# Kernel optimization log

Hardware: AMD Instinct MI355X
Metric: run time of the kernel (lower is better)

## Reference

```python
import jax, jax.numpy as jnp
import numpy as np

MAX_REL_POS = 1024


def rel_to_abs(x):
    """Music Transformer skew: [b,h,l,l] rel logits -> abs-position logits."""
    b, h, l, _ = x.shape
    x = jnp.pad(x, ((0, 0), (0, 0), (0, 0), (1, 0)))  # pad left of last dim
    x = x.reshape(b, h, l + 1, l)
    return x[:, :, 1:l + 1, :l]


def get_rel_embeddings(embed, seq_len):
    m = embed.shape[0]
    pad_len = max(seq_len - m, 0)
    start = max(m - seq_len, 0)
    padded = jnp.pad(embed, ((pad_len, 0), (0, 0)))
    return padded[start:, :]  # [seq_len, d]


def setup_inputs() -> dict:
    key = jax.random.key(0)
    kq, kk, kv, kr = jax.random.split(key, 4)
    B, H, L, D = 2, 8, 2048, 64
    # scale q so logits are O(1) (realistic attention magnitudes)
    q = jax.random.normal(kq, (B, H, L, D), dtype=jnp.float32) * (1.0 / np.sqrt(D))
    k = jax.random.normal(kk, (B, H, L, D), dtype=jnp.float32)
    v = jax.random.normal(kv, (B, H, L, D), dtype=jnp.float32)
    rel_keys_weight = jax.random.normal(kr, (MAX_REL_POS, D), dtype=jnp.float32)
    # causal mask: True = masked (masked_fill semantics)
    mask = jnp.triu(jnp.ones((L, L), dtype=bool), k=1)[None, None]
    return {"q": q, "k": k, "v": v, "rel_keys_weight": rel_keys_weight, "mask": mask}


def reference(q, k, v, rel_keys_weight, mask):
    L = q.shape[2]
    logits = jnp.einsum('bhqd,bhkd->bhqk', q, k)
    rel_keys = get_rel_embeddings(rel_keys_weight, L)          # [L, D]
    rel_logits = jnp.einsum('bhqd,md->bhqm', q, rel_keys)      # [B,H,L,L]
    logits = logits + rel_to_abs(rel_logits)
    logits = jnp.where(mask, -jnp.inf, logits)
    weights = jax.nn.softmax(logits, axis=3)
    output = jnp.matmul(weights, v)
    return (output, weights)
```

## Files before the change

kernel.cpp:

```cpp
#include <hip/hip_runtime.h>
#include <hip/hip_bf16.h>

typedef short bf16x8 __attribute__((ext_vector_type(8)));
typedef float f32x4  __attribute__((ext_vector_type(4)));

#define SEQ  2048
#define HD   64
#define LDT  72
#define TSTR 84
#define PSTR 72
#define OUT0 (16 * SEQ * HD)

__device__ __forceinline__ short f2bf(float x) {
    unsigned u = __float_as_uint(x);
    unsigned r = u + 0x7fffu + ((u >> 16) & 1u);
    return (short)(r >> 16);
}
__device__ __forceinline__ float bf2f(short s) {
    return __uint_as_float(((unsigned)(unsigned short)s) << 16);
}

__device__ __forceinline__ void stage64(const float* __restrict__ src_base,
                                        short* __restrict__ dst, int tid) {
    const int r = tid >> 2, cg = tid & 3;
    const float4* src = (const float4*)(src_base + (size_t)r * HD + cg * 16);
    float f[16];
#pragma unroll
    for (int t = 0; t < 4; ++t) {
        float4 v4 = src[t];
        f[4*t] = v4.x; f[4*t+1] = v4.y; f[4*t+2] = v4.z; f[4*t+3] = v4.w;
    }
    bf16x8 p0, p1;
#pragma unroll
    for (int t = 0; t < 8; ++t) { p0[t] = f2bf(f[t]); p1[t] = f2bf(f[t+8]); }
    *(bf16x8*)&dst[r * LDT + cg * 16]     = p0;
    *(bf16x8*)&dst[r * LDT + cg * 16 + 8] = p1;
}

__device__ __forceinline__ void stageG(const float* __restrict__ eg,
                                       short* __restrict__ Gs, int tid, int i0, int j0) {
    const int dd = tid >> 1, hf = tid & 1;
    const int e = 1086 - i0 + j0 - dd;
    short* dst = &Gs[dd * LDT + hf * 32];
    if (e >= 0 && e < 1024) {
        const float4* src = (const float4*)(eg + (size_t)e * HD + hf * 32);
#pragma unroll
        for (int u = 0; u < 4; ++u) {
            float4 a = src[2*u], b = src[2*u + 1];
            bf16x8 p;
            p[0] = f2bf(a.x); p[1] = f2bf(a.y); p[2] = f2bf(a.z); p[3] = f2bf(a.w);
            p[4] = f2bf(b.x); p[5] = f2bf(b.y); p[6] = f2bf(b.z); p[7] = f2bf(b.w);
            *(bf16x8*)&dst[u * 8] = p;
        }
    } else {
        bf16x8 z = {0,0,0,0,0,0,0,0};
#pragma unroll
        for (int u = 0; u < 4; ++u) *(bf16x8*)&dst[u * 8] = z;
    }
}

__device__ __forceinline__ void compute_sc(const bf16x8* aq, const short* __restrict__ Ks,
                                           const short* __restrict__ Gs, short* __restrict__ Tw,
                                           int wv, int qd, int c, int i0, int j0, f32x4* sc) {
    f32x4 tc[5];
    const f32x4 zz = {0.f, 0.f, 0.f, 0.f};
#pragma unroll
    for (int ct = 0; ct < 4; ++ct) sc[ct] = zz;
#pragma unroll
    for (int dt = 0; dt < 5; ++dt) tc[dt] = zz;
#pragma unroll
    for (int s = 0; s < 2; ++s) {
        bf16x8 a = aq[s];
#pragma unroll
        for (int ct = 0; ct < 4; ++ct) {
            bf16x8 b = *(const bf16x8*)&Ks[(ct * 16 + c) * LDT + s * 32 + qd * 8];
            sc[ct] = __builtin_amdgcn_mfma_f32_16x16x32_bf16(a, b, sc[ct], 0, 0, 0);
        }
#pragma unroll
        for (int dt = 0; dt < 5; ++dt) {
            bf16x8 g = *(const bf16x8*)&Gs[((wv + dt) * 16 + c) * LDT + s * 32 + qd * 8];
            tc[dt] = __builtin_amdgcn_mfma_f32_16x16x32_bf16(a, g, tc[dt], 0, 0, 0);
        }
    }
#pragma unroll
    for (int dt = 0; dt < 5; ++dt)
#pragma unroll
        for (int rg = 0; rg < 4; ++rg)
            Tw[(qd * 4 + rg) * TSTR + dt * 16 + c] = f2bf(tc[dt][rg]);
#pragma unroll
    for (int ct = 0; ct < 4; ++ct)
#pragma unroll
        for (int rg = 0; rg < 4; ++rg) {
            const int rl  = qd * 4 + rg;
            const int ddl = rl + 63 - ct * 16 - c;
            float sval = sc[ct][rg] + bf2f(Tw[rl * TSTR + ddl]);
            const int ig = i0 + wv * 16 + rl;
            const int jg = j0 + ct * 16 + c;
            sc[ct][rg] = (jg <= ig) ? sval : -3.0e38f;
        }
}

__global__ __launch_bounds__(256, 2)
void relattn(const float* __restrict__ qg, const float* __restrict__ kg,
             const float* __restrict__ vg, const float* __restrict__ eg,
             float* __restrict__ outp)
{
    __shared__ short Qs[64 * LDT];
    __shared__ short Ks[64 * LDT];
    __shared__ short Vt[64 * LDT];
    __shared__ short Gs[128 * LDT];
    __shared__ short TP[4 * 16 * TSTR];

    const int tid  = threadIdx.x;
    const int wv   = tid >> 6;
    const int lane = tid & 63;
    const int qd   = lane >> 4;
    const int c    = lane & 15;

    const int bh = blockIdx.x & 15;
    const int qt = 31 - (blockIdx.x >> 4);
    const int i0 = qt * 64;

    float* Wg = outp + OUT0;

    {
        const int z0v = (qt + 1) * 16;
        for (int r = 0; r < 64; ++r) {
            float4* dst = (float4*)(Wg + ((size_t)(bh * SEQ + i0 + r)) * SEQ);
            for (int jv = z0v + tid; jv < SEQ / 4; jv += 256)
                dst[jv] = make_float4(0.f, 0.f, 0.f, 0.f);
        }
    }

    stage64(qg + ((size_t)(bh * SEQ + i0)) * HD, Qs, tid);
    __syncthreads();
    bf16x8 aq[2];
#pragma unroll
    for (int s = 0; s < 2; ++s)
        aq[s] = *(const bf16x8*)&Qs[(wv * 16 + c) * LDT + s * 32 + qd * 8];

    short* Tw = &TP[wv * 16 * TSTR];

    float mrun[4], lrun[4];
#pragma unroll
    for (int rg = 0; rg < 4; ++rg) { mrun[rg] = -3.0e38f; lrun[rg] = 0.f; }

    for (int kt = 0; kt <= qt; ++kt) {
        const int j0 = kt * 64;
        __syncthreads();
        stage64(kg + ((size_t)(bh * SEQ + j0)) * HD, Ks, tid);
        stageG(eg, Gs, tid, i0, j0);
        __syncthreads();

        f32x4 sc[4];
        compute_sc(aq, Ks, Gs, Tw, wv, qd, c, i0, j0, sc);

#pragma unroll
        for (int rg = 0; rg < 4; ++rg) {
            float mx = fmaxf(fmaxf(sc[0][rg], sc[1][rg]), fmaxf(sc[2][rg], sc[3][rg]));
            mx = fmaxf(mx, __shfl_xor(mx, 1));
            mx = fmaxf(mx, __shfl_xor(mx, 2));
            mx = fmaxf(mx, __shfl_xor(mx, 4));
            mx = fmaxf(mx, __shfl_xor(mx, 8));
            const float mnew = fmaxf(mrun[rg], mx);
            float ss = __expf(sc[0][rg] - mnew) + __expf(sc[1][rg] - mnew)
                     + __expf(sc[2][rg] - mnew) + __expf(sc[3][rg] - mnew);
            ss += __shfl_xor(ss, 1);
            ss += __shfl_xor(ss, 2);
            ss += __shfl_xor(ss, 4);
            ss += __shfl_xor(ss, 8);
            lrun[rg] = lrun[rg] * __expf(mrun[rg] - mnew) + ss;
            mrun[rg] = mnew;
        }
    }

    float linv[4];
#pragma unroll
    for (int rg = 0; rg < 4; ++rg) linv[rg] = 1.0f / lrun[rg];

    f32x4 ob[4];
    {
        const f32x4 zz = {0.f, 0.f, 0.f, 0.f};
#pragma unroll
        for (int dt = 0; dt < 4; ++dt) ob[dt] = zz;
    }

    for (int kt = 0; kt <= qt; ++kt) {
        const int j0 = kt * 64;
        __syncthreads();
        stage64(kg + ((size_t)(bh * SEQ + j0)) * HD, Ks, tid);
        stageG(eg, Gs, tid, i0, j0);
        {
            const int r = tid >> 2, cg = tid & 3;
            const float4* src = (const float4*)(vg + ((size_t)(bh * SEQ + j0 + r)) * HD + cg * 16);
            float f[16];
#pragma unroll
            for (int t = 0; t < 4; ++t) {
                float4 v4 = src[t];
                f[4*t] = v4.x; f[4*t+1] = v4.y; f[4*t+2] = v4.z; f[4*t+3] = v4.w;
            }
#pragma unroll
            for (int t = 0; t < 16; ++t) Vt[(cg * 16 + t) * LDT + r] = f2bf(f[t]);
        }
        __syncthreads();

        f32x4 sc[4];
        compute_sc(aq, Ks, Gs, Tw, wv, qd, c, i0, j0, sc);

#pragma unroll
        for (int rg = 0; rg < 4; ++rg) {
            const int rl = qd * 4 + rg;
            const int ig = i0 + wv * 16 + rl;
            float* wrow = Wg + ((size_t)(bh * SEQ + ig)) * SEQ + j0;
#pragma unroll
            for (int ct = 0; ct < 4; ++ct) {
                const float w = __expf(sc[ct][rg] - mrun[rg]) * linv[rg];
                wrow[ct * 16 + c] = w;
                Tw[rl * PSTR + ct * 16 + c] = f2bf(w);
            }
        }

#pragma unroll
        for (int s = 0; s < 2; ++s) {
            bf16x8 ap = *(const bf16x8*)&Tw[c * PSTR + s * 32 + qd * 8];
#pragma unroll
            for (int dt = 0; dt < 4; ++dt) {
                bf16x8 bv = *(const bf16x8*)&Vt[(dt * 16 + c) * LDT + s * 32 + qd * 8];
                ob[dt] = __builtin_amdgcn_mfma_f32_16x16x32_bf16(ap, bv, ob[dt], 0, 0, 0);
            }
        }
    }

#pragma unroll
    for (int dt = 0; dt < 4; ++dt)
#pragma unroll
        for (int rg = 0; rg < 4; ++rg) {
            const int ig = i0 + wv * 16 + qd * 4 + rg;
            outp[((size_t)(bh * SEQ + ig)) * HD + dt * 16 + c] = ob[dt][rg];
        }
}

extern "C" void kernel_launch(void* const* d_in, const int* in_sizes, int n_in,
                              void* d_out, int out_size, void* d_ws, size_t ws_size,
                              hipStream_t stream) {
    const float* q = (const float*)d_in[0];
    const float* k = (const float*)d_in[1];
    const float* v = (const float*)d_in[2];
    const float* e = (const float*)d_in[3];
    float* out = (float*)d_out;
    hipLaunchKernelGGL(relattn, dim3(512), dim3(256), 0, stream, q, k, v, e, out);
}
```

Before: 453.4 us.

## Precompute bf16 K/V^T/rel-embedding buffers and read operands directly from global

Adds a prep kernel that converts K, transposed V, and a padded rel-embedding table to bf16 in workspace. The attention kernel then drops its shared-memory staging and barriers and loads MFMA operands straight from global/L2. The skew of the relative logits is done with lane shuffles instead of a shared-memory round trip. The running max is removed and exp is taken without subtracting it, which relies on logits staying O(1). The q-tile order is changed to interleave long and short tiles across blocks. This risks overflow for large logits and uncoalesced global reads in exchange for fewer syncs and less LDS traffic.

```diff
diff --git a/kernel.cpp b/kernel.cpp
--- a/kernel.cpp
+++ b/kernel.cpp
@@ -1,115 +1,122 @@
 #include <hip/hip_runtime.h>
-#include <hip/hip_bf16.h>
 
 typedef short bf16x8 __attribute__((ext_vector_type(8)));
 typedef float f32x4  __attribute__((ext_vector_type(4)));
 
-#define SEQ  2048
-#define HD   64
-#define LDT  72
-#define TSTR 84
-#define PSTR 72
-#define OUT0 (16 * SEQ * HD)
+#define SEQ   2048
+#define HD    64
+#define OUT0  (16 * SEQ * HD)
+#define KB_OFF 0
+#define VT_OFF (16 * SEQ * HD)
+#define GT_OFF (2 * 16 * SEQ * HD)
+#define GPAD  1056
+#define GNR   2208
+#define PSTR  72
 
 __device__ __forceinline__ short f2bf(float x) {
     unsigned u = __float_as_uint(x);
     unsigned r = u + 0x7fffu + ((u >> 16) & 1u);
     return (short)(r >> 16);
 }
-__device__ __forceinline__ float bf2f(short s) {
-    return __uint_as_float(((unsigned)(unsigned short)s) << 16);
-}
-
-__device__ __forceinline__ void stage64(const float* __restrict__ src_base,
-                                        short* __restrict__ dst, int tid) {
-    const int r = tid >> 2, cg = tid & 3;
-    const float4* src = (const float4*)(src_base + (size_t)r * HD + cg * 16);
-    float f[16];
-#pragma unroll
-    for (int t = 0; t < 4; ++t) {
-        float4 v4 = src[t];
-        f[4*t] = v4.x; f[4*t+1] = v4.y; f[4*t+2] = v4.z; f[4*t+3] = v4.w;
-    }
-    bf16x8 p0, p1;
-#pragma unroll
-    for (int t = 0; t < 8; ++t) { p0[t] = f2bf(f[t]); p1[t] = f2bf(f[t+8]); }
-    *(bf16x8*)&dst[r * LDT + cg * 16]     = p0;
-    *(bf16x8*)&dst[r * LDT + cg * 16 + 8] = p1;
-}
-
-__device__ __forceinline__ void stageG(const float* __restrict__ eg,
-                                       short* __restrict__ Gs, int tid, int i0, int j0) {
-    const int dd = tid >> 1, hf = tid & 1;
-    const int e = 1086 - i0 + j0 - dd;
-    short* dst = &Gs[dd * LDT + hf * 32];
-    if (e >= 0 && e < 1024) {
-        const float4* src = (const float4*)(eg + (size_t)e * HD + hf * 32);
+__device__ __forceinline__ void cvt8(const float4& x, const float4& y, bf16x8& p) {
+    p[0] = f2bf(x.x); p[1] = f2bf(x.y); p[2] = f2bf(x.z); p[3] = f2bf(x.w);
+    p[4] = f2bf(y.x); p[5] = f2bf(y.y); p[6] = f2bf(y.z); p[7] = f2bf(y.w);
+}
+
+__global__ __launch_bounds__(256)
+void prep(const float* __restrict__ kg, const float* __restrict__ vg,
+          const float* __restrict__ eg, short* __restrict__ ws)
+{
+    const int b = blockIdx.x, t = threadIdx.x;
+    short* Kb = ws + KB_OFF;
+    short* Vt = ws + VT_OFF;
+    short* Gt = ws + GT_OFF;
+    if (b < 512) {
+        __shared__ short tile[64 * 72];
+        const int bh = b >> 5, kb = b & 31;
+        const int r = t >> 2, cg = t & 3;
+        const float4* src = (const float4*)(vg + ((size_t)(bh * SEQ + kb * 64 + r)) * HD + cg * 16);
+        bf16x8 p0, p1;
+        cvt8(src[0], src[1], p0);
+        cvt8(src[2], src[3], p1);
+        *(bf16x8*)&tile[r * 72 + cg * 16]     = p0;
+        *(bf16x8*)&tile[r * 72 + cg * 16 + 8] = p1;
+        __syncthreads();
+        const int d = t >> 2, kq = t & 3;
+#pragma unroll
+        for (int u = 0; u < 2; ++u) {
+            bf16x8 q;
+#pragma unroll
+            for (int x = 0; x < 8; ++x) q[x] = tile[(kq * 16 + u * 8 + x) * 72 + d];
+            *(bf16x8*)&Vt[((size_t)(bh * 64 + d)) * SEQ + kb * 64 + kq * 16 + u * 8] = q;
+        }
+    } else if (b < 768) {
+        const int idx = (b - 512) * 256 + t;
+        const float4* src = (const float4*)kg + (size_t)idx * 8;
+        short* dst = Kb + (size_t)idx * 32;
 #pragma unroll
         for (int u = 0; u < 4; ++u) {
-            float4 a = src[2*u], b = src[2*u + 1];
-            bf16x8 p;
-            p[0] = f2bf(a.x); p[1] = f2bf(a.y); p[2] = f2bf(a.z); p[3] = f2bf(a.w);
-            p[4] = f2bf(b.x); p[5] = f2bf(b.y); p[6] = f2bf(b.z); p[7] = f2bf(b.w);
+            bf16x8 p; cvt8(src[2 * u], src[2 * u + 1], p);
             *(bf16x8*)&dst[u * 8] = p;
         }
     } else {
-        bf16x8 z = {0,0,0,0,0,0,0,0};
-#pragma unroll
-        for (int u = 0; u < 4; ++u) *(bf16x8*)&dst[u * 8] = z;
-    }
-}
-
-__device__ __forceinline__ void compute_sc(const bf16x8* aq, const short* __restrict__ Ks,
-                                           const short* __restrict__ Gs, short* __restrict__ Tw,
-                                           int wv, int qd, int c, int i0, int j0, f32x4* sc) {
+        for (int i = (b - 768) * 256 + t; i < GNR * HD; i += 64 * 256) {
+            const int g = i >> 6, d = i & 63;
+            const int e = g - GPAD;
+            Gt[i] = (e >= 0 && e < 1024) ? f2bf(eg[(size_t)e * HD + d]) : (short)0;
+        }
+    }
+}
+
+__device__ __forceinline__ void compute_sc(const bf16x8* aq, const short* __restrict__ Kb,
+                                           const short* __restrict__ Gt,
+                                           int j0, int iw, int qd, int c, int lane,
+                                           f32x4* sc, bool diag, int dloc)
+{
     f32x4 tc[5];
     const f32x4 zz = {0.f, 0.f, 0.f, 0.f};
 #pragma unroll
     for (int ct = 0; ct < 4; ++ct) sc[ct] = zz;
 #pragma unroll
     for (int dt = 0; dt < 5; ++dt) tc[dt] = zz;
+    const short* kbase = Kb + ((size_t)(j0 + c)) * HD + qd * 8;
+    const short* gbase = Gt + ((size_t)(2142 + j0 - iw - c)) * HD + qd * 8;
 #pragma unroll
     for (int s = 0; s < 2; ++s) {
         bf16x8 a = aq[s];
 #pragma unroll
         for (int ct = 0; ct < 4; ++ct) {
-            bf16x8 b = *(const bf16x8*)&Ks[(ct * 16 + c) * LDT + s * 32 + qd * 8];
+            bf16x8 b = *(const bf16x8*)&kbase[(ct * 16) * HD + s * 32];
             sc[ct] = __builtin_amdgcn_mfma_f32_16x16x32_bf16(a, b, sc[ct], 0, 0, 0);
         }
 #pragma unroll
         for (int dt = 0; dt < 5; ++dt) {
-            bf16x8 g = *(const bf16x8*)&Gs[((wv + dt) * 16 + c) * LDT + s * 32 + qd * 8];
+            bf16x8 g = *(const bf16x8*)&gbase[-(dt * 16) * HD + s * 32];
             tc[dt] = __builtin_amdgcn_mfma_f32_16x16x32_bf16(a, g, tc[dt], 0, 0, 0);
         }
     }
 #pragma unroll
-    for (int dt = 0; dt < 5; ++dt)
-#pragma unroll
-        for (int rg = 0; rg < 4; ++rg)
-            Tw[(qd * 4 + rg) * TSTR + dt * 16 + c] = f2bf(tc[dt][rg]);
-#pragma unroll
-    for (int ct = 0; ct < 4; ++ct)
-#pragma unroll
-        for (int rg = 0; rg < 4; ++rg) {
-            const int rl  = qd * 4 + rg;
-            const int ddl = rl + 63 - ct * 16 - c;
-            float sval = sc[ct][rg] + bf2f(Tw[rl * TSTR + ddl]);
-            const int ig = i0 + wv * 16 + rl;
-            const int jg = j0 + ct * 16 + c;
-            sc[ct][rg] = (jg <= ig) ? sval : -3.0e38f;
-        }
+    for (int rg = 0; rg < 4; ++rg) {
+        const int rl  = qd * 4 + rg;
+        const int cp  = (rl + 63 - c) & 15;
+        const int src = (lane & 48) | cp;
+        const bool hi = (rl + 63 - cp) >= 64;
+#pragma unroll
+        for (int ct = 0; ct < 4; ++ct) {
+            float vs = hi ? tc[4 - ct][rg] : tc[3 - ct][rg];
+            float tr = __shfl(vs, src, 64);
+            float sval = sc[ct][rg] + tr;
+            if (diag && (ct * 16 + c > dloc + rl)) sval = -3.0e38f;
+            sc[ct][rg] = sval;
+        }
+    }
 }
 
 __global__ __launch_bounds__(256, 2)
-void relattn(const float* __restrict__ qg, const float* __restrict__ kg,
-             const float* __restrict__ vg, const float* __restrict__ eg,
+void relattn(const float* __restrict__ qg, const short* __restrict__ ws,
              float* __restrict__ outp)
 {
-    __shared__ short Qs[64 * LDT];
-    __shared__ short Ks[64 * LDT];
-    __shared__ short Vt[64 * LDT];
-    __shared__ short Gs[128 * LDT];
-    __shared__ short TP[4 * 16 * TSTR];
+    __shared__ short Ps[4 * 16 * PSTR];
 
     const int tid  = threadIdx.x;
     const int wv   = tid >> 6;
@@ -118,9 +125,14 @@
     const int c    = lane & 15;
 
     const int bh = blockIdx.x & 15;
-    const int qt = 31 - (blockIdx.x >> 4);
+    const int u  = blockIdx.x >> 4;
+    const int qt = (u < 16) ? (31 - u) : (u - 16);
     const int i0 = qt * 64;
-
+    const int iw = i0 + wv * 16;
+
+    const short* Kb = ws + KB_OFF + (size_t)bh * SEQ * HD;
+    const short* Vt = ws + VT_OFF + (size_t)bh * 64 * SEQ;
+    const short* Gt = ws + GT_OFF;
     float* Wg = outp + OUT0;
 
     {
@@ -132,51 +144,37 @@
         }
     }
 
-    stage64(qg + ((size_t)(bh * SEQ + i0)) * HD, Qs, tid);
-    __syncthreads();
     bf16x8 aq[2];
-#pragma unroll
-    for (int s = 0; s < 2; ++s)
-        aq[s] = *(const bf16x8*)&Qs[(wv * 16 + c) * LDT + s * 32 + qd * 8];
-
-    short* Tw = &TP[wv * 16 * TSTR];
-
-    float mrun[4], lrun[4];
-#pragma unroll
-    for (int rg = 0; rg < 4; ++rg) { mrun[rg] = -3.0e38f; lrun[rg] = 0.f; }
-
+    {
+        const float* qrow = qg + ((size_t)(bh * SEQ + iw + c)) * HD;
+#pragma unroll
+        for (int s = 0; s < 2; ++s) {
+            float4 x = *(const float4*)(qrow + s * 32 + qd * 8);
+            float4 y = *(const float4*)(qrow + s * 32 + qd * 8 + 4);
+            cvt8(x, y, aq[s]);
+        }
+    }
+
+    float lrun[4];
+#pragma unroll
+    for (int rg = 0; rg < 4; ++rg) lrun[rg] = 0.f;
     for (int kt = 0; kt <= qt; ++kt) {
-        const int j0 = kt * 64;
-        __syncthreads();
-        stage64(kg + ((size_t)(bh * SEQ + j0)) * HD, Ks, tid);
-        stageG(eg, Gs, tid, i0, j0);
-        __syncthreads();
-
         f32x4 sc[4];
-        compute_sc(aq, Ks, Gs, Tw, wv, qd, c, i0, j0, sc);
-
-#pragma unroll
-        for (int rg = 0; rg < 4; ++rg) {
-            float mx = fmaxf(fmaxf(sc[0][rg], sc[1][rg]), fmaxf(sc[2][rg], sc[3][rg]));
-            mx = fmaxf(mx, __shfl_xor(mx, 1));
-            mx = fmaxf(mx, __shfl_xor(mx, 2));
-            mx = fmaxf(mx, __shfl_xor(mx, 4));
-            mx = fmaxf(mx, __shfl_xor(mx, 8));
-            const float mnew = fmaxf(mrun[rg], mx);
-            float ss = __expf(sc[0][rg] - mnew) + __expf(sc[1][rg] - mnew)
-                     + __expf(sc[2][rg] - mnew) + __expf(sc[3][rg] - mnew);
-            ss += __shfl_xor(ss, 1);
-            ss += __shfl_xor(ss, 2);
-            ss += __shfl_xor(ss, 4);
-            ss += __shfl_xor(ss, 8);
-            lrun[rg] = lrun[rg] * __expf(mrun[rg] - mnew) + ss;
-            mrun[rg] = mnew;
-        }
-    }
-
-    float linv[4];
-#pragma unroll
-    for (int rg = 0; rg < 4; ++rg) linv[rg] = 1.0f / lrun[rg];
+        compute_sc(aq, Kb, Gt, kt * 64, iw, qd, c, lane, sc, kt == qt, wv * 16);
+#pragma unroll
+        for (int rg = 0; rg < 4; ++rg)
+            lrun[rg] += (__expf(sc[0][rg]) + __expf(sc[1][rg]))
+                      + (__expf(sc[2][rg]) + __expf(sc[3][rg]));
+    }
+#pragma unroll
+    for (int rg = 0; rg < 4; ++rg) {
+        float ss = lrun[rg];
+        ss += __shfl_xor(ss, 1);
+        ss += __shfl_xor(ss, 2);
+        ss += __shfl_xor(ss, 4);
+        ss += __shfl_xor(ss, 8);
+        lrun[rg] = 1.0f / ss;
+    }
 
     f32x4 ob[4];
     {
@@ -184,48 +182,30 @@
 #pragma unroll
         for (int dt = 0; dt < 4; ++dt) ob[dt] = zz;
     }
-
+    short* Pw = &Ps[wv * 16 * PSTR];
     for (int kt = 0; kt <= qt; ++kt) {
         const int j0 = kt * 64;
-        __syncthreads();
-        stage64(kg + ((size_t)(bh * SEQ + j0)) * HD, Ks, tid);
-        stageG(eg, Gs, tid, i0, j0);
-        {
-            const int r = tid >> 2, cg = tid & 3;
-            const float4* src = (const float4*)(vg + ((size_t)(bh * SEQ + j0 + r)) * HD + cg * 16);
-            float f[16];
-#pragma unroll
-            for (int t = 0; t < 4; ++t) {
-                float4 v4 = src[t];
-                f[4*t] = v4.x; f[4*t+1] = v4.y; f[4*t+2] = v4.z; f[4*t+3] = v4.w;
-            }
-#pragma unroll
-            for (int t = 0; t < 16; ++t) Vt[(cg * 16 + t) * LDT + r] = f2bf(f[t]);
-        }
-        __syncthreads();
-
         f32x4 sc[4];
-        compute_sc(aq, Ks, Gs, Tw, wv, qd, c, i0, j0, sc);
+        compute_sc(aq, Kb, Gt, j0, iw, qd, c, lane, sc, kt == qt, wv * 16);
 
 #pragma unroll
         for (int rg = 0; rg < 4; ++rg) {
             const int rl = qd * 4 + rg;
-            const int ig = i0 + wv * 16 + rl;
-            float* wrow = Wg + ((size_t)(bh * SEQ + ig)) * SEQ + j0;
+            float* wrow = Wg + ((size_t)(bh * SEQ + iw + rl)) * SEQ + j0;
 #pragma unroll
             for (int ct = 0; ct < 4; ++ct) {
-                const float w = __expf(sc[ct][rg] - mrun[rg]) * linv[rg];
+                const float w = __expf(sc[ct][rg]) * lrun[rg];
                 wrow[ct * 16 + c] = w;
-                Tw[rl * PSTR + ct * 16 + c] = f2bf(w);
+                Pw[rl * PSTR + ct * 16 + c] = f2bf(w);
             }
         }
 
 #pragma unroll
         for (int s = 0; s < 2; ++s) {
-            bf16x8 ap = *(const bf16x8*)&Tw[c * PSTR + s * 32 + qd * 8];
+            bf16x8 ap = *(const bf16x8*)&Pw[c * PSTR + s * 32 + qd * 8];
 #pragma unroll
             for (int dt = 0; dt < 4; ++dt) {
-                bf16x8 bv = *(const bf16x8*)&Vt[(dt * 16 + c) * LDT + s * 32 + qd * 8];
+                bf16x8 bv = *(const bf16x8*)&Vt[((size_t)(dt * 16 + c)) * SEQ + j0 + s * 32 + qd * 8];
                 ob[dt] = __builtin_amdgcn_mfma_f32_16x16x32_bf16(ap, bv, ob[dt], 0, 0, 0);
             }
         }
@@ -234,10 +214,8 @@
 #pragma unroll
     for (int dt = 0; dt < 4; ++dt)
 #pragma unroll
-        for (int rg = 0; rg < 4; ++rg) {
-            const int ig = i0 + wv * 16 + qd * 4 + rg;
-            outp[((size_t)(bh * SEQ + ig)) * HD + dt * 16 + c] = ob[dt][rg];
-        }
+        for (int rg = 0; rg < 4; ++rg)
+            outp[((size_t)(bh * SEQ + iw + qd * 4 + rg)) * HD + dt * 16 + c] = ob[dt][rg];
 }
 
 extern "C" void kernel_launch(void* const* d_in, const int* in_sizes, int n_in,
@@ -248,5 +226,7 @@
     const float* v = (const float*)d_in[2];
     const float* e = (const float*)d_in[3];
     float* out = (float*)d_out;
-    hipLaunchKernelGGL(relattn, dim3(512), dim3(256), 0, stream, q, k, v, e, out);
-}
+    short* ws = (short*)d_ws;
+    hipLaunchKernelGGL(prep,    dim3(832), dim3(256), 0, stream, k, v, e, ws);
+    hipLaunchKernelGGL(relattn, dim3(512), dim3(256), 0, stream, q, ws, out);
+}
```

Measured after the change: 518.3 us. 14.3% more time.
